# Performance work log

Hardware: AMD Instinct MI355X
Metric: run time of the kernel (lower is better)

Reference implementation:

```python
import jax, jax.numpy as jnp
import numpy as np

# hyperparameters (match init_kwargs / AF3 atom transformer)
B, N, C, CP = 1, 2048, 128, 16      # batch, n_atom, c_atom, c_atom_pair
H, D = 4, 32                        # heads, head dim
HD = H * D                          # 128
NB = 3                              # no_blocks
TC = 2 * C                          # n_transition * c_atom
NQ, NK = 32, 128                    # n_query, n_key
INF = 1.0e9


def _ln(x, g=None, b=None):
    m = jnp.mean(x, axis=-1, keepdims=True)
    v = jnp.mean((x - m) ** 2, axis=-1, keepdims=True)
    y = (x - m) * jax.lax.rsqrt(v + 1e-5)
    if g is not None:
        y = y * g
    if b is not None:
        y = y + b
    return y


def _adaln(a, s, gamma, wsig, bsig, wskip):
    # AF3 Algorithm 26: AdaLN(a, s)
    an = _ln(a)                     # no affine
    sn = _ln(s, gamma)              # scale only
    return jax.nn.sigmoid(sn @ wsig + bsig) * an + sn @ wskip


def _neighborhood_beta():
    # compute_neighborhood_mask with create_sparsity_mask=False
    n_center = N // NQ + 1
    centers = (NQ / 2 - 0.5) + jnp.arange(n_center, dtype=jnp.float32) * NQ
    l = jnp.arange(N, dtype=jnp.float32)
    row = (jnp.abs(l[:, None] - centers[None, :]) < NQ / 2).astype(jnp.float32)
    col = (jnp.abs(l[:, None] - centers[None, :]) < NK / 2).astype(jnp.float32)
    beta = row @ col.T              # [N, N], in {0,1} since query windows are disjoint
    return (beta - 1.0) * INF       # 0 where attended, -inf elsewhere


def setup_inputs() -> dict:
    key = jax.random.key(0)
    it = iter(jax.random.split(key, 64))
    def rn(shape, s=0.02):
        return jax.random.normal(next(it), shape, jnp.float32) * s
    inp = dict(
        ql=rn((B, N, C), 1.0),
        cl=rn((B, N, C), 1.0),
        plm=rn((B, N, N, CP), 1.0),
        atom_mask=jnp.ones((B, N), jnp.float32),
        # per-block stacked params, leading dim NB
        attn_gamma=1.0 + rn((NB, C)), attn_wsig=rn((NB, C, C)),
        attn_bsig=rn((NB, C)), attn_wskip=rn((NB, C, C)),
        wq=rn((NB, C, HD)), bq=rn((NB, HD)), wk=rn((NB, C, HD)), wv=rn((NB, C, HD)),
        lnz_g=1.0 + rn((NB, CP)), lnz_b=rn((NB, CP)), w_pair=rn((NB, CP, H)),
        w_gate=rn((NB, C, HD)), w_out=rn((NB, HD, C)),
        w_ao=rn((NB, C, C)), b_ao=rn((NB, C)) - 2.0,
        tr_gamma=1.0 + rn((NB, C)), tr_wsig=rn((NB, C, C)),
        tr_bsig=rn((NB, C)), tr_wskip=rn((NB, C, C)),
        w_t1=rn((NB, C, TC)), w_t2=rn((NB, C, TC)), w_t3=rn((NB, TC, C)),
        w_to=rn((NB, C, C)), b_to=rn((NB, C)) - 2.0,
    )
    return inp


def reference(ql, cl, plm, atom_mask,
              attn_gamma, attn_wsig, attn_bsig, attn_wskip,
              wq, bq, wk, wv, lnz_g, lnz_b, w_pair,
              w_gate, w_out, w_ao, b_ao,
              tr_gamma, tr_wsig, tr_bsig, tr_wskip,
              w_t1, w_t2, w_t3, w_to, b_to):
    beta = _neighborhood_beta()                       # [N, N]
    mask_bias = (atom_mask - 1.0) * INF               # [B, N]
    scale = 1.0 / np.sqrt(D)
    a, s = ql, cl
    for i in range(NB):
        # --- AttentionPairBias with AdaLN (AF3 Alg. 24) ---
        an = _adaln(a, s, attn_gamma[i], attn_wsig[i], attn_bsig[i], attn_wskip[i])
        q = (an @ wq[i] + bq[i]).reshape(B, N, H, D)
        k = (an @ wk[i]).reshape(B, N, H, D)
        v = (an @ wv[i]).reshape(B, N, H, D)
        pb = _ln(plm, lnz_g[i], lnz_b[i]) @ w_pair[i]  # [B, N, N, H]
        logits = (jnp.einsum('bqhd,bkhd->bhqk', q, k) * scale
                  + pb.transpose(0, 3, 1, 2)
                  + beta[None, None]
                  + mask_bias[:, None, None, :])
        attn = jax.nn.softmax(logits, axis=-1)
        o = jnp.einsum('bhqk,bkhd->bqhd', attn, v)
        g = jax.nn.sigmoid(an @ w_gate[i]).reshape(B, N, H, D)
        o = (g * o).reshape(B, N, HD) @ w_out[i]
        b_attn = jax.nn.sigmoid(s @ w_ao[i] + b_ao[i]) * o   # adaLN-zero output gate
        # --- ConditionedTransitionBlock (AF3 Alg. 25) on old a ---
        tn = _adaln(a, s, tr_gamma[i], tr_wsig[i], tr_bsig[i], tr_wskip[i])
        t = jax.nn.silu(tn @ w_t1[i]) * (tn @ w_t2[i])       # SwiGLU
        t = jax.nn.sigmoid(s @ w_to[i] + b_to[i]) * (t @ w_t3[i])
        a = b_attn + t                                       # AF3 Alg. 23
    return a
```

## Files before the change

kernel.cpp:

```cpp
#include <hip/hip_runtime.h>
#include <math.h>

#define NA 2048
#define CD 128
#define NC ((size_t)262144)

typedef unsigned short u16;
typedef short s8v __attribute__((ext_vector_type(8)));
typedef float f4v __attribute__((ext_vector_type(4)));

__device__ __forceinline__ float sigm(float x) { return 1.f / (1.f + __expf(-x)); }

__device__ __forceinline__ u16 f2bf(float x) {
    unsigned u = __float_as_uint(x);
    u += 0x7fffu + ((u >> 16) & 1u);
    return (u16)(u >> 16);
}
__device__ __forceinline__ float bf2f(u16 h) { return __uint_as_float((unsigned)h << 16); }

__global__ __launch_bounds__(256)
void prep_w(const float* __restrict__ attn_gamma, const float* __restrict__ attn_wsig,
            const float* __restrict__ attn_bsig, const float* __restrict__ attn_wskip,
            const float* __restrict__ wq, const float* __restrict__ wk,
            const float* __restrict__ wv, const float* __restrict__ w_gate,
            const float* __restrict__ w_out, const float* __restrict__ w_ao,
            const float* __restrict__ b_ao,
            const float* __restrict__ tr_gamma, const float* __restrict__ tr_wsig,
            const float* __restrict__ tr_bsig, const float* __restrict__ tr_wskip,
            const float* __restrict__ w_t1, const float* __restrict__ w_t2,
            const float* __restrict__ w_t3, const float* __restrict__ w_to,
            const float* __restrict__ b_to,
            u16* __restrict__ BP1h, u16* __restrict__ BP1l,
            u16* __restrict__ BG1h, u16* __restrict__ BG1l,
            u16* __restrict__ BG2h, u16* __restrict__ BG2l,
            float* __restrict__ Pbias) {
    int e = blockIdx.x * 256 + threadIdx.x;
    if (e >= 835584) {
        int t = e - 835584;
        if (t < 2304) {
            int z = t / 768, rem = t % 768, j = rem >> 7, c = rem & 127;
            float v = 0.f;
            if (j == 0) v = attn_bsig[z * 128 + c];
            else if (j == 2) v = tr_bsig[z * 128 + c];
            else if (j == 4) v = b_ao[z * 128 + c];
            else if (j == 5) v = b_to[z * 128 + c];
            Pbias[t] = v;
        }
        return;
    }
    int z = e / 278528, r = e % 278528;
    float val;
    u16 *dh, *dl;
    size_t dofs;
    if (r < 98304) {
        int c = r >> 7, k = r & 127, seg = c >> 7, cc = c & 127;
        const float* w;
        const float* g = nullptr;
        switch (seg) {
            case 0: w = attn_wsig; g = attn_gamma; break;
            case 1: w = attn_wskip; g = attn_gamma; break;
            case 2: w = tr_wsig; g = tr_gamma; break;
            case 3: w = tr_wskip; g = tr_gamma; break;
            case 4: w = w_ao; break;
            default: w = w_to; break;
        }
        val = w[((size_t)z * 128 + k) * 128 + cc];
        if (g) val *= g[z * 128 + k];
        dh = BP1h; dl = BP1l; dofs = (size_t)z * 98304 + r;
    } else if (r < 229376) {
        int t = r - 98304, c = t >> 7, k = t & 127;
        if (c < 512) {
            int seg = c >> 7, cc = c & 127;
            const float* w = (seg == 0) ? wq : (seg == 1) ? wk : (seg == 2) ? wv : w_gate;
            val = w[((size_t)z * 128 + k) * 128 + cc];
        } else {
            int tt = c - 512;
            const float* w = (tt < 256) ? w_t1 : w_t2;
            val = w[(size_t)z * 32768 + (size_t)k * 256 + (tt & 255)];
        }
        dh = BG1h; dl = BG1l; dofs = (size_t)z * 131072 + t;
    } else {
        int t = r - 229376, c = t / 384, k = t % 384;
        val = (k < 128) ? w_out[((size_t)z * 128 + k) * 128 + c]
                        : w_t3[(size_t)z * 32768 + (size_t)(k - 128) * 128 + c];
        dh = BG2h; dl = BG2l; dofs = (size_t)z * 49152 + t;
    }
    u16 h = f2bf(val);
    dh[dofs] = h;
    dl[dofs] = f2bf(val - bf2f(h));
}

__global__ __launch_bounds__(256)
void ln_split(const float* __restrict__ cl, u16* __restrict__ lnsh, u16* __restrict__ lnsl,
              u16* __restrict__ clh, u16* __restrict__ cll) {
    int row = blockIdx.x * 4 + (threadIdx.x >> 6);
    int lane = threadIdx.x & 63;
    size_t idx = (size_t)row * CD + lane * 2;
    float2 v = *(const float2*)(cl + idx);
    float s = v.x + v.y, sq = v.x * v.x + v.y * v.y;
#pragma unroll
    for (int m = 1; m < 64; m <<= 1) { s += __shfl_xor(s, m); sq += __shfl_xor(sq, m); }
    float mean = s * (1.f / 128.f);
    float var = sq * (1.f / 128.f) - mean * mean;
    float r = 1.f / sqrtf(var + 1e-5f);
    float lx = (v.x - mean) * r, ly = (v.y - mean) * r;
    ushort2 h, l;
    h.x = f2bf(lx); h.y = f2bf(ly);
    l.x = f2bf(lx - bf2f(h.x)); l.y = f2bf(ly - bf2f(h.y));
    *(ushort2*)(lnsh + idx) = h; *(ushort2*)(lnsl + idx) = l;
    h.x = f2bf(v.x); h.y = f2bf(v.y);
    l.x = f2bf(v.x - bf2f(h.x)); l.y = f2bf(v.y - bf2f(h.y));
    *(ushort2*)(clh + idx) = h; *(ushort2*)(cll + idx) = l;
}

__global__ __launch_bounds__(256)
void an_tn(const float* __restrict__ a, const float* __restrict__ sg,
           u16* __restrict__ anh, u16* __restrict__ anl,
           u16* __restrict__ tnh, u16* __restrict__ tnl) {
    int row = blockIdx.x * 4 + (threadIdx.x >> 6);
    int lane = threadIdx.x & 63;
    size_t idx = (size_t)row * CD + lane * 2;
    float2 v = *(const float2*)(a + idx);
    float s = v.x + v.y, sq = v.x * v.x + v.y * v.y;
#pragma unroll
    for (int m = 1; m < 64; m <<= 1) { s += __shfl_xor(s, m); sq += __shfl_xor(sq, m); }
    float mean = s * (1.f / 128.f);
    float var = sq * (1.f / 128.f) - mean * mean;
    float r = 1.f / sqrtf(var + 1e-5f);
    float lx = (v.x - mean) * r, ly = (v.y - mean) * r;
    float2 s0 = *(const float2*)(sg + idx);
    float2 s1 = *(const float2*)(sg + NC + idx);
    float2 s2 = *(const float2*)(sg + 2 * NC + idx);
    float2 s3 = *(const float2*)(sg + 3 * NC + idx);
    float ax = fmaf(s0.x, lx, s1.x), ay = fmaf(s0.y, ly, s1.y);
    float tx = fmaf(s2.x, lx, s3.x), ty = fmaf(s2.y, ly, s3.y);
    ushort2 h, l;
    h.x = f2bf(ax); h.y = f2bf(ay);
    l.x = f2bf(ax - bf2f(h.x)); l.y = f2bf(ay - bf2f(h.y));
    *(ushort2*)(anh + idx) = h; *(ushort2*)(anl + idx) = l;
    h.x = f2bf(tx); h.y = f2bf(ty);
    l.x = f2bf(tx - bf2f(h.x)); l.y = f2bf(ty - bf2f(h.y));
    *(ushort2*)(tnh + idx) = h; *(ushort2*)(tnl + idx) = l;
}

__device__ __forceinline__ void mf_core(const u16* __restrict__ Ah, const u16* __restrict__ Al,
                                        int AK, int kA,
                                        const u16* __restrict__ Bh, const u16* __restrict__ Bl,
                                        int BK, int kB,
                                        int r0, int c0, int nks, f4v (&acc)[2][2]) {
    const int lane = threadIdx.x & 63;
    const int lr = lane & 15;
    const int kg = (lane >> 4) << 3;
    const u16* pa = Ah + (size_t)(r0 + lr) * AK + kA + kg;
    const u16* pal = Al + (size_t)(r0 + lr) * AK + kA + kg;
    const u16* pb = Bh + (size_t)(c0 + lr) * BK + kB + kg;
    const u16* pbl = Bl + (size_t)(c0 + lr) * BK + kB + kg;
    const size_t aS = (size_t)16 * AK, bS = (size_t)16 * BK;
#pragma unroll
    for (int ks = 0; ks < nks; ++ks) {
        const int ko = ks * 32;
        s8v a0h = *(const s8v*)(pa + ko);
        s8v a1h = *(const s8v*)(pa + aS + ko);
        s8v a0l = *(const s8v*)(pal + ko);
        s8v a1l = *(const s8v*)(pal + aS + ko);
        s8v b0h = *(const s8v*)(pb + ko);
        s8v b1h = *(const s8v*)(pb + bS + ko);
        s8v b0l = *(const s8v*)(pbl + ko);
        s8v b1l = *(const s8v*)(pbl + bS + ko);
        acc[0][0] = __builtin_amdgcn_mfma_f32_16x16x32_bf16(a0h, b0h, acc[0][0], 0, 0, 0);
        acc[0][1] = __builtin_amdgcn_mfma_f32_16x16x32_bf16(a0h, b1h, acc[0][1], 0, 0, 0);
        acc[1][0] = __builtin_amdgcn_mfma_f32_16x16x32_bf16(a1h, b0h, acc[1][0], 0, 0, 0);
        acc[1][1] = __builtin_amdgcn_mfma_f32_16x16x32_bf16(a1h, b1h, acc[1][1], 0, 0, 0);
        acc[0][0] = __builtin_amdgcn_mfma_f32_16x16x32_bf16(a0h, b0l, acc[0][0], 0, 0, 0);
        acc[0][1] = __builtin_amdgcn_mfma_f32_16x16x32_bf16(a0h, b1l, acc[0][1], 0, 0, 0);
        acc[1][0] = __builtin_amdgcn_mfma_f32_16x16x32_bf16(a1h, b0l, acc[1][0], 0, 0, 0);
        acc[1][1] = __builtin_amdgcn_mfma_f32_16x16x32_bf16(a1h, b1l, acc[1][1], 0, 0, 0);
        acc[0][0] = __builtin_amdgcn_mfma_f32_16x16x32_bf16(a0l, b0h, acc[0][0], 0, 0, 0);
        acc[0][1] = __builtin_amdgcn_mfma_f32_16x16x32_bf16(a0l, b1h, acc[0][1], 0, 0, 0);
        acc[1][0] = __builtin_amdgcn_mfma_f32_16x16x32_bf16(a1l, b0h, acc[1][0], 0, 0, 0);
        acc[1][1] = __builtin_amdgcn_mfma_f32_16x16x32_bf16(a1l, b1h, acc[1][1], 0, 0, 0);
    }
}

__global__ __launch_bounds__(256)
void mf_p1(const u16* __restrict__ lnsh, const u16* __restrict__ lnsl,
           const u16* __restrict__ clh, const u16* __restrict__ cll,
           const u16* __restrict__ BP1h, const u16* __restrict__ BP1l,
           const float* __restrict__ Pbias, float* __restrict__ sg) {
    const int z = blockIdx.z, chunk = blockIdx.y;
    const int r0 = blockIdx.x * 32;
    const int c0 = (threadIdx.x >> 6) * 32;
    const u16* Ah = (chunk < 4) ? lnsh : clh;
    const u16* Al = (chunk < 4) ? lnsl : cll;
    const size_t bo = (size_t)z * 98304 + (size_t)chunk * 16384;
    f4v acc[2][2] = {};
    mf_core(Ah, Al, 128, 0, BP1h + bo, BP1l + bo, 128, 0, r0, c0, 4, acc);
    const bool dosig = (chunk != 1) && (chunk != 3);
    const float* bp = Pbias + (z * 6 + chunk) * 128;
    float* dst = sg + ((size_t)z * 6 + chunk) * NC;
    const int lane = threadIdx.x & 63;
    const int lr = lane & 15, rb = (lane >> 4) * 4;
#pragma unroll
    for (int mi = 0; mi < 2; ++mi)
#pragma unroll
        for (int i = 0; i < 4; ++i) {
            int row = r0 + mi * 16 + rb + i;
#pragma unroll
            for (int ni = 0; ni < 2; ++ni) {
                int col = c0 + ni * 16 + lr;
                float x = acc[mi][ni][i];
                if (dosig) x = sigm(x + bp[col]);
                dst[(size_t)row * CD + col] = x;
            }
        }
}

__global__ __launch_bounds__(256)
void mf_g1(const u16* __restrict__ anh, const u16* __restrict__ anl,
           const u16* __restrict__ tnh, const u16* __restrict__ tnl,
           const u16* __restrict__ Bh, const u16* __restrict__ Bl,
           const float* __restrict__ bq, float* __restrict__ qkvg, float* __restrict__ tbuf) {
    const int chunk = blockIdx.y;
    const int r0 = blockIdx.x * 32;
    const int c0 = (threadIdx.x >> 6) * 32;
    const u16* Ah = (chunk < 4) ? anh : tnh;
    const u16* Al = (chunk < 4) ? anl : tnl;
    const size_t bo = (size_t)chunk * 16384;
    f4v acc[2][2] = {};
    mf_core(Ah, Al, 128, 0, Bh + bo, Bl + bo, 128, 0, r0, c0, 4, acc);
    float* dst;
    int cb;
    if (chunk < 4) { dst = qkvg; cb = chunk * 128; } else { dst = tbuf; cb = (chunk - 4) * 128; }
    const int lane = threadIdx.x & 63;
    const int lr = lane & 15, rb = (lane >> 4) * 4;
#pragma unroll
    for (int mi = 0; mi < 2; ++mi)
#pragma unroll
        for (int i = 0; i < 4; ++i) {
            int row = r0 + mi * 16 + rb + i;
#pragma unroll
            for (int ni = 0; ni < 2; ++ni) {
                int col = c0 + ni * 16 + lr;
                float x = acc[mi][ni][i];
                if (chunk == 0) x += bq[col];
                dst[(size_t)row * 512 + cb + col] = x;
            }
        }
}

__global__ __launch_bounds__(256)
void mf_g2(const u16* __restrict__ ogh, const u16* __restrict__ ogl,
           const u16* __restrict__ swh, const u16* __restrict__ swl,
           const u16* __restrict__ Bh, const u16* __restrict__ Bl,
           const float* __restrict__ sg4, const float* __restrict__ sg5,
           float* __restrict__ dst) {
    const int r0 = blockIdx.x * 32;
    const int c0 = (threadIdx.x >> 6) * 32;
    f4v acc1[2][2] = {}, acc2[2][2] = {};
    mf_core(ogh, ogl, 128, 0, Bh, Bl, 384, 0, r0, c0, 4, acc1);
    mf_core(swh, swl, 256, 0, Bh, Bl, 384, 128, r0, c0, 8, acc2);
    const int lane = threadIdx.x & 63;
    const int lr = lane & 15, rb = (lane >> 4) * 4;
#pragma unroll
    for (int mi = 0; mi < 2; ++mi)
#pragma unroll
        for (int i = 0; i < 4; ++i) {
            int row = r0 + mi * 16 + rb + i;
#pragma unroll
            for (int ni = 0; ni < 2; ++ni) {
                int col = c0 + ni * 16 + lr;
                size_t idx = (size_t)row * CD + col;
                dst[idx] = sg4[idx] * acc1[mi][ni][i] + sg5[idx] * acc2[mi][ni][i];
            }
        }
}

__global__ __launch_bounds__(256)
void pb_kernel(const float* __restrict__ plm, const float* __restrict__ lnz_g,
               const float* __restrict__ lnz_b, const float* __restrict__ w_pair,
               float* __restrict__ pb) {
    __shared__ float gw[3][4][16];
    __shared__ float c0[3][4];
    int t = threadIdx.x;
    if (t < 12) {
        int i = t >> 2, h = t & 3;
        float c = 0.f;
        for (int cp = 0; cp < 16; ++cp) {
            float wp = w_pair[(i * 16 + cp) * 4 + h];
            gw[i][h][cp] = lnz_g[i * 16 + cp] * wp;
            c += lnz_b[i * 16 + cp] * wp;
        }
        c0[i][h] = c;
    }
    __syncthreads();
    int c = blockIdx.x;
    int p = blockIdx.y * 256 + t;
    int ql = p >> 7, kl = p & 127;
    int kstart = max(0, c * 32 - 48), kend = min(2048, c * 32 + 80);
    int k = kstart + kl;
    if (k >= kend) return;
    int q = c * 32 + ql;
    const float* row = plm + ((size_t)q * 2048 + (size_t)k) * 16;
    float x[16];
#pragma unroll
    for (int j = 0; j < 4; ++j) {
        float4 v = *(const float4*)(row + j * 4);
        x[j * 4 + 0] = v.x; x[j * 4 + 1] = v.y; x[j * 4 + 2] = v.z; x[j * 4 + 3] = v.w;
    }
    float s = 0.f, sq = 0.f;
#pragma unroll
    for (int cp = 0; cp < 16; ++cp) { s += x[cp]; sq += x[cp] * x[cp]; }
    float mean = s * (1.f / 16.f);
    float var = sq * (1.f / 16.f) - mean * mean;
    float r = 1.f / sqrtf(var + 1e-5f);
    float xn[16];
#pragma unroll
    for (int cp = 0; cp < 16; ++cp) xn[cp] = (x[cp] - mean) * r;
#pragma unroll
    for (int i = 0; i < 3; ++i)
#pragma unroll
        for (int h = 0; h < 4; ++h) {
            float d = c0[i][h];
#pragma unroll
            for (int cp = 0; cp < 16; ++cp) d = fmaf(xn[cp], gw[i][h][cp], d);
            pb[((((size_t)i * 64 + c) * 4 + h) * 32 + ql) * 128 + kl] = d;
        }
}

__global__ __launch_bounds__(256)
void attn_sw(const float* __restrict__ qkvg, const float* __restrict__ pb,
             const float* __restrict__ atom_mask, const float* __restrict__ tbuf,
             u16* __restrict__ ogh, u16* __restrict__ ogl,
             u16* __restrict__ swh, u16* __restrict__ swl) {
    const int c = blockIdx.x;
    const int tid = threadIdx.x;
    if (blockIdx.y >= 4) {
        const int r0 = c * 32;
        const int cb = (blockIdx.y - 4) * 128 + (tid & 31) * 4;
#pragma unroll
        for (int p = 0; p < 4; ++p) {
            int r = r0 + p * 8 + (tid >> 5);
            float4 x1 = *(const float4*)(tbuf + (size_t)r * 512 + cb);
            float4 x2 = *(const float4*)(tbuf + (size_t)r * 512 + 256 + cb);
            float4 s;
            s.x = x1.x * sigm(x1.x) * x2.x;
            s.y = x1.y * sigm(x1.y) * x2.y;
            s.z = x1.z * sigm(x1.z) * x2.z;
            s.w = x1.w * sigm(x1.w) * x2.w;
            size_t o = (size_t)r * 256 + cb;
            ushort4 h, l;
            h.x = f2bf(s.x); l.x = f2bf(s.x - bf2f(h.x));
            h.y = f2bf(s.y); l.y = f2bf(s.y - bf2f(h.y));
            h.z = f2bf(s.z); l.z = f2bf(s.z - bf2f(h.z));
            h.w = f2bf(s.w); l.w = f2bf(s.w - bf2f(h.w));
            *(ushort4*)(swh + o) = h;
            *(ushort4*)(swl + o) = l;
        }
        return;
    }
    const int h = blockIdx.y;
    const int kstart = max(0, c * 32 - 48);
    const int kend = min(2048, c * 32 + 80);
    const int nk = kend - kstart;

    __shared__ float Kt[128 * 36];
    __shared__ float Vt[128 * 36];
    __shared__ float Qs[32 * 36];
    __shared__ float Ps[32 * 132];

    {
        int q = tid >> 3, dq = tid & 7;
        float4 v = *(const float4*)(qkvg + (size_t)(c * 32 + q) * 512 + h * 32 + dq * 4);
        *(float4*)(Qs + q * 36 + dq * 4) = v;
    }
#pragma unroll
    for (int it = 0; it < 4; ++it) {
        int idx = it * 256 + tid;
        int kl = idx >> 3, dq = idx & 7;
        float4 kv = make_float4(0.f, 0.f, 0.f, 0.f);
        float4 vv = make_float4(0.f, 0.f, 0.f, 0.f);
        if (kl < nk) {
            size_t base = (size_t)(kstart + kl) * 512 + h * 32 + dq * 4;
            kv = *(const float4*)(qkvg + base + 128);
            vv = *(const float4*)(qkvg + base + 256);
        }
        int sw = (kl >> 4) & 7;
        *(float4*)(Kt + kl * 36 + ((dq ^ sw) << 2)) = kv;
        *(float4*)(Vt + kl * 36 + (dq << 2)) = vv;
    }
    __syncthreads();

    {
        const int qp = tid >> 4;
        const int ks = tid & 15;
        const int q0r = qp * 2, q1r = qp * 2 + 1;
        float4 qa[8], qb[8];
#pragma unroll
        for (int dq = 0; dq < 8; ++dq) {
            qa[dq] = *(const float4*)(Qs + q0r * 36 + dq * 4);
            qb[dq] = *(const float4*)(Qs + q1r * 36 + dq * 4);
        }
        const float* pbp = pb + ((size_t)(c * 4 + h) * 32) * 128;
        float lg0[8], lg1[8];
#pragma unroll
        for (int ki = 0; ki < 8; ++ki) {
            int kl = ks * 8 + ki;
            int sw = (kl >> 4) & 7;
            float d0 = 0.f, d1 = 0.f;
#pragma unroll
            for (int dq = 0; dq < 8; ++dq) {
                float4 kv = *(const float4*)(Kt + kl * 36 + ((dq ^ sw) << 2));
                d0 += qa[dq].x * kv.x + qa[dq].y * kv.y + qa[dq].z * kv.z + qa[dq].w * kv.w;
                d1 += qb[dq].x * kv.x + qb[dq].y * kv.y + qb[dq].z * kv.z + qb[dq].w * kv.w;
            }
            if (kl < nk) {
                int k = kstart + kl;
                float mb = (atom_mask[k] - 1.f) * 1.0e9f;
                lg0[ki] = fmaf(d0, 0.17677669529663687f, pbp[(size_t)q0r * 128 + kl] + mb);
                lg1[ki] = fmaf(d1, 0.17677669529663687f, pbp[(size_t)q1r * 128 + kl] + mb);
            } else {
                lg0[ki] = -1e30f;
                lg1[ki] = -1e30f;
            }
        }
        float m0 = lg0[0], m1 = lg1[0];
#pragma unroll
        for (int ki = 1; ki < 8; ++ki) { m0 = fmaxf(m0, lg0[ki]); m1 = fmaxf(m1, lg1[ki]); }
#pragma unroll
        for (int msk = 1; msk < 16; msk <<= 1) {
            m0 = fmaxf(m0, __shfl_xor(m0, msk));
            m1 = fmaxf(m1, __shfl_xor(m1, msk));
        }
        float s0 = 0.f, s1 = 0.f;
#pragma unroll
        for (int ki = 0; ki < 8; ++ki) {
            lg0[ki] = __expf(lg0[ki] - m0); s0 += lg0[ki];
            lg1[ki] = __expf(lg1[ki] - m1); s1 += lg1[ki];
        }
#pragma unroll
        for (int msk = 1; msk < 16; msk <<= 1) {
            s0 += __shfl_xor(s0, msk);
            s1 += __shfl_xor(s1, msk);
        }
        float i0 = 1.f / s0, i1 = 1.f / s1;
        float4 w;
        w.x = lg0[0] * i0; w.y = lg0[1] * i0; w.z = lg0[2] * i0; w.w = lg0[3] * i0;
        *(float4*)(Ps + q0r * 132 + ks * 8) = w;
        w.x = lg0[4] * i0; w.y = lg0[5] * i0; w.z = lg0[6] * i0; w.w = lg0[7] * i0;
        *(float4*)(Ps + q0r * 132 + ks * 8 + 4) = w;
        w.x = lg1[0] * i1; w.y = lg1[1] * i1; w.z = lg1[2] * i1; w.w = lg1[3] * i1;
        *(float4*)(Ps + q1r * 132 + ks * 8) = w;
        w.x = lg1[4] * i1; w.y = lg1[5] * i1; w.z = lg1[6] * i1; w.w = lg1[7] * i1;
        *(float4*)(Ps + q1r * 132 + ks * 8 + 4) = w;
    }
    __syncthreads();
    {
        const int q = tid >> 3;
        const int ds = tid & 7;
        float o0 = 0.f, o1 = 0.f, o2 = 0.f, o3 = 0.f;
#pragma unroll 4
        for (int kl = 0; kl < nk; ++kl) {
            float p = Ps[q * 132 + kl];
            float4 vv = *(const float4*)(Vt + kl * 36 + ds * 4);
            o0 = fmaf(p, vv.x, o0); o1 = fmaf(p, vv.y, o1);
            o2 = fmaf(p, vv.z, o2); o3 = fmaf(p, vv.w, o3);
        }
        size_t gl = (size_t)(c * 32 + q) * 512 + 384 + h * 32 + ds * 4;
        float4 g = *(const float4*)(qkvg + gl);
        float4 ov;
        ov.x = o0 * sigm(g.x); ov.y = o1 * sigm(g.y);
        ov.z = o2 * sigm(g.z); ov.w = o3 * sigm(g.w);
        size_t oidx = (size_t)(c * 32 + q) * 128 + h * 32 + ds * 4;
        ushort4 hh, ll;
        hh.x = f2bf(ov.x); ll.x = f2bf(ov.x - bf2f(hh.x));
        hh.y = f2bf(ov.y); ll.y = f2bf(ov.y - bf2f(hh.y));
        hh.z = f2bf(ov.z); ll.z = f2bf(ov.z - bf2f(hh.z));
        hh.w = f2bf(ov.w); ll.w = f2bf(ov.w - bf2f(hh.w));
        *(ushort4*)(ogh + oidx) = hh;
        *(ushort4*)(ogl + oidx) = ll;
    }
}

extern "C" void kernel_launch(void* const* d_in, const int* in_sizes, int n_in,
                              void* d_out, int out_size, void* d_ws, size_t ws_size,
                              hipStream_t stream) {
    const float* ql = (const float*)d_in[0];
    const float* cl = (const float*)d_in[1];
    const float* plm = (const float*)d_in[2];
    const float* atom_mask = (const float*)d_in[3];
    const float* attn_gamma = (const float*)d_in[4];
    const float* attn_wsig = (const float*)d_in[5];
    const float* attn_bsig = (const float*)d_in[6];
    const float* attn_wskip = (const float*)d_in[7];
    const float* wq = (const float*)d_in[8];
    const float* bq = (const float*)d_in[9];
    const float* wk = (const float*)d_in[10];
    const float* wv = (const float*)d_in[11];
    const float* lnz_g = (const float*)d_in[12];
    const float* lnz_b = (const float*)d_in[13];
    const float* w_pair = (const float*)d_in[14];
    const float* w_gate = (const float*)d_in[15];
    const float* w_out = (const float*)d_in[16];
    const float* w_ao = (const float*)d_in[17];
    const float* b_ao = (const float*)d_in[18];
    const float* tr_gamma = (const float*)d_in[19];
    const float* tr_wsig = (const float*)d_in[20];
    const float* tr_bsig = (const float*)d_in[21];
    const float* tr_wskip = (const float*)d_in[22];
    const float* w_t1 = (const float*)d_in[23];
    const float* w_t2 = (const float*)d_in[24];
    const float* w_t3 = (const float*)d_in[25];
    const float* w_to = (const float*)d_in[26];
    const float* b_to = (const float*)d_in[27];
    float* out = (float*)d_out;
    float* ws = (float*)d_ws;

    float* sg = ws;
    float* qkvg = ws + 18 * NC;
    float* tbuf = ws + 22 * NC;
    float* pb = ws + 26 * NC;
    float* a_buf = ws + 38 * NC;
    float* Pbias = ws + 39 * NC;
    u16* us = (u16*)(ws + 40 * NC);
    u16* lnsh = us;             u16* lnsl = us + NC;
    u16* clh = us + 2 * NC;     u16* cll = us + 3 * NC;
    u16* anh = us + 4 * NC;     u16* anl = us + 5 * NC;
    u16* tnh = us + 6 * NC;     u16* tnl = us + 7 * NC;
    u16* ogh = us + 8 * NC;     u16* ogl = us + 9 * NC;
    u16* swh = us + 10 * NC;    u16* swl = us + 12 * NC;
    u16* BP1h = us + 14 * NC;
    u16* BP1l = BP1h + 294912;
    u16* BG1h = BP1l + 294912;
    u16* BG1l = BG1h + 393216;
    u16* BG2h = BG1l + 393216;
    u16* BG2l = BG2h + 147456;

    prep_w<<<3273, 256, 0, stream>>>(attn_gamma, attn_wsig, attn_bsig, attn_wskip,
        wq, wk, wv, w_gate, w_out, w_ao, b_ao,
        tr_gamma, tr_wsig, tr_bsig, tr_wskip,
        w_t1, w_t2, w_t3, w_to, b_to,
        BP1h, BP1l, BG1h, BG1l, BG2h, BG2l, Pbias);
    ln_split<<<NA / 4, 256, 0, stream>>>(cl, lnsh, lnsl, clh, cll);
    mf_p1<<<dim3(64, 6, 3), 256, 0, stream>>>(lnsh, lnsl, clh, cll, BP1h, BP1l, Pbias, sg);
    pb_kernel<<<dim3(64, 16), 256, 0, stream>>>(plm, lnz_g, lnz_b, w_pair, pb);

    for (int i = 0; i < 3; ++i) {
        const float* a_cur = (i == 0) ? ql : a_buf;
        float* sgi = sg + (size_t)i * 6 * NC;
        an_tn<<<NA / 4, 256, 0, stream>>>(a_cur, sgi, anh, anl, tnh, tnl);
        mf_g1<<<dim3(64, 8), 256, 0, stream>>>(anh, anl, tnh, tnl,
            BG1h + (size_t)i * 131072, BG1l + (size_t)i * 131072,
            bq + (size_t)i * 128, qkvg, tbuf);
        attn_sw<<<dim3(64, 6), 256, 0, stream>>>(qkvg,
            pb + (size_t)i * 64 * 4 * 32 * 128, atom_mask, tbuf, ogh, ogl, swh, swl);
        float* dst = (i == 2) ? out : a_buf;
        mf_g2<<<64, 256, 0, stream>>>(ogh, ogl, swh, swl,
            BG2h + (size_t)i * 49152, BG2l + (size_t)i * 49152,
            sgi + 4 * NC, sgi + 5 * NC, dst);
    }
}
```

Before: 163.4 us.

## Fuse LayerNorm into GEMMs, move attention to MFMA, fuse SwiGLU into output GEMM

Folds the LayerNorm/AdaLN and bf16 hi/lo split into the GEMM kernels through swizzled LDS staging, removing the separate ln_split and an_tn passes. Attention is rewritten to use MFMA on bf16-split Q and transposed V, and the SwiGLU product is computed inside the output GEMM. pb_kernel now writes zeros for out-of-range keys. A hipMemsetAsync of the whole workspace is added each call, which brings extra memory traffic.

```diff
diff --git a/kernel.cpp b/kernel.cpp
--- a/kernel.cpp
+++ b/kernel.cpp
@@ -8,9 +8,9 @@
 typedef unsigned short u16;
 typedef short s8v __attribute__((ext_vector_type(8)));
 typedef float f4v __attribute__((ext_vector_type(4)));
+#define MFMA __builtin_amdgcn_mfma_f32_16x16x32_bf16
 
 __device__ __forceinline__ float sigm(float x) { return 1.f / (1.f + __expf(-x)); }
-
 __device__ __forceinline__ u16 f2bf(float x) {
     unsigned u = __float_as_uint(x);
     u += 0x7fffu + ((u >> 16) & 1u);
@@ -91,196 +91,11 @@
 }
 
 __global__ __launch_bounds__(256)
-void ln_split(const float* __restrict__ cl, u16* __restrict__ lnsh, u16* __restrict__ lnsl,
-              u16* __restrict__ clh, u16* __restrict__ cll) {
-    int row = blockIdx.x * 4 + (threadIdx.x >> 6);
-    int lane = threadIdx.x & 63;
-    size_t idx = (size_t)row * CD + lane * 2;
-    float2 v = *(const float2*)(cl + idx);
-    float s = v.x + v.y, sq = v.x * v.x + v.y * v.y;
-#pragma unroll
-    for (int m = 1; m < 64; m <<= 1) { s += __shfl_xor(s, m); sq += __shfl_xor(sq, m); }
-    float mean = s * (1.f / 128.f);
-    float var = sq * (1.f / 128.f) - mean * mean;
-    float r = 1.f / sqrtf(var + 1e-5f);
-    float lx = (v.x - mean) * r, ly = (v.y - mean) * r;
-    ushort2 h, l;
-    h.x = f2bf(lx); h.y = f2bf(ly);
-    l.x = f2bf(lx - bf2f(h.x)); l.y = f2bf(ly - bf2f(h.y));
-    *(ushort2*)(lnsh + idx) = h; *(ushort2*)(lnsl + idx) = l;
-    h.x = f2bf(v.x); h.y = f2bf(v.y);
-    l.x = f2bf(v.x - bf2f(h.x)); l.y = f2bf(v.y - bf2f(h.y));
-    *(ushort2*)(clh + idx) = h; *(ushort2*)(cll + idx) = l;
-}
-
-__global__ __launch_bounds__(256)
-void an_tn(const float* __restrict__ a, const float* __restrict__ sg,
-           u16* __restrict__ anh, u16* __restrict__ anl,
-           u16* __restrict__ tnh, u16* __restrict__ tnl) {
-    int row = blockIdx.x * 4 + (threadIdx.x >> 6);
-    int lane = threadIdx.x & 63;
-    size_t idx = (size_t)row * CD + lane * 2;
-    float2 v = *(const float2*)(a + idx);
-    float s = v.x + v.y, sq = v.x * v.x + v.y * v.y;
-#pragma unroll
-    for (int m = 1; m < 64; m <<= 1) { s += __shfl_xor(s, m); sq += __shfl_xor(sq, m); }
-    float mean = s * (1.f / 128.f);
-    float var = sq * (1.f / 128.f) - mean * mean;
-    float r = 1.f / sqrtf(var + 1e-5f);
-    float lx = (v.x - mean) * r, ly = (v.y - mean) * r;
-    float2 s0 = *(const float2*)(sg + idx);
-    float2 s1 = *(const float2*)(sg + NC + idx);
-    float2 s2 = *(const float2*)(sg + 2 * NC + idx);
-    float2 s3 = *(const float2*)(sg + 3 * NC + idx);
-    float ax = fmaf(s0.x, lx, s1.x), ay = fmaf(s0.y, ly, s1.y);
-    float tx = fmaf(s2.x, lx, s3.x), ty = fmaf(s2.y, ly, s3.y);
-    ushort2 h, l;
-    h.x = f2bf(ax); h.y = f2bf(ay);
-    l.x = f2bf(ax - bf2f(h.x)); l.y = f2bf(ay - bf2f(h.y));
-    *(ushort2*)(anh + idx) = h; *(ushort2*)(anl + idx) = l;
-    h.x = f2bf(tx); h.y = f2bf(ty);
-    l.x = f2bf(tx - bf2f(h.x)); l.y = f2bf(ty - bf2f(h.y));
-    *(ushort2*)(tnh + idx) = h; *(ushort2*)(tnl + idx) = l;
-}
-
-__device__ __forceinline__ void mf_core(const u16* __restrict__ Ah, const u16* __restrict__ Al,
-                                        int AK, int kA,
-                                        const u16* __restrict__ Bh, const u16* __restrict__ Bl,
-                                        int BK, int kB,
-                                        int r0, int c0, int nks, f4v (&acc)[2][2]) {
-    const int lane = threadIdx.x & 63;
-    const int lr = lane & 15;
-    const int kg = (lane >> 4) << 3;
-    const u16* pa = Ah + (size_t)(r0 + lr) * AK + kA + kg;
-    const u16* pal = Al + (size_t)(r0 + lr) * AK + kA + kg;
-    const u16* pb = Bh + (size_t)(c0 + lr) * BK + kB + kg;
-    const u16* pbl = Bl + (size_t)(c0 + lr) * BK + kB + kg;
-    const size_t aS = (size_t)16 * AK, bS = (size_t)16 * BK;
-#pragma unroll
-    for (int ks = 0; ks < nks; ++ks) {
-        const int ko = ks * 32;
-        s8v a0h = *(const s8v*)(pa + ko);
-        s8v a1h = *(const s8v*)(pa + aS + ko);
-        s8v a0l = *(const s8v*)(pal + ko);
-        s8v a1l = *(const s8v*)(pal + aS + ko);
-        s8v b0h = *(const s8v*)(pb + ko);
-        s8v b1h = *(const s8v*)(pb + bS + ko);
-        s8v b0l = *(const s8v*)(pbl + ko);
-        s8v b1l = *(const s8v*)(pbl + bS + ko);
-        acc[0][0] = __builtin_amdgcn_mfma_f32_16x16x32_bf16(a0h, b0h, acc[0][0], 0, 0, 0);
-        acc[0][1] = __builtin_amdgcn_mfma_f32_16x16x32_bf16(a0h, b1h, acc[0][1], 0, 0, 0);
-        acc[1][0] = __builtin_amdgcn_mfma_f32_16x16x32_bf16(a1h, b0h, acc[1][0], 0, 0, 0);
-        acc[1][1] = __builtin_amdgcn_mfma_f32_16x16x32_bf16(a1h, b1h, acc[1][1], 0, 0, 0);
-        acc[0][0] = __builtin_amdgcn_mfma_f32_16x16x32_bf16(a0h, b0l, acc[0][0], 0, 0, 0);
-        acc[0][1] = __builtin_amdgcn_mfma_f32_16x16x32_bf16(a0h, b1l, acc[0][1], 0, 0, 0);
-        acc[1][0] = __builtin_amdgcn_mfma_f32_16x16x32_bf16(a1h, b0l, acc[1][0], 0, 0, 0);
-        acc[1][1] = __builtin_amdgcn_mfma_f32_16x16x32_bf16(a1h, b1l, acc[1][1], 0, 0, 0);
-        acc[0][0] = __builtin_amdgcn_mfma_f32_16x16x32_bf16(a0l, b0h, acc[0][0], 0, 0, 0);
-        acc[0][1] = __builtin_amdgcn_mfma_f32_16x16x32_bf16(a0l, b1h, acc[0][1], 0, 0, 0);
-        acc[1][0] = __builtin_amdgcn_mfma_f32_16x16x32_bf16(a1l, b0h, acc[1][0], 0, 0, 0);
-        acc[1][1] = __builtin_amdgcn_mfma_f32_16x16x32_bf16(a1l, b1h, acc[1][1], 0, 0, 0);
-    }
-}
-
-__global__ __launch_bounds__(256)
-void mf_p1(const u16* __restrict__ lnsh, const u16* __restrict__ lnsl,
-           const u16* __restrict__ clh, const u16* __restrict__ cll,
-           const u16* __restrict__ BP1h, const u16* __restrict__ BP1l,
-           const float* __restrict__ Pbias, float* __restrict__ sg) {
-    const int z = blockIdx.z, chunk = blockIdx.y;
-    const int r0 = blockIdx.x * 32;
-    const int c0 = (threadIdx.x >> 6) * 32;
-    const u16* Ah = (chunk < 4) ? lnsh : clh;
-    const u16* Al = (chunk < 4) ? lnsl : cll;
-    const size_t bo = (size_t)z * 98304 + (size_t)chunk * 16384;
-    f4v acc[2][2] = {};
-    mf_core(Ah, Al, 128, 0, BP1h + bo, BP1l + bo, 128, 0, r0, c0, 4, acc);
-    const bool dosig = (chunk != 1) && (chunk != 3);
-    const float* bp = Pbias + (z * 6 + chunk) * 128;
-    float* dst = sg + ((size_t)z * 6 + chunk) * NC;
-    const int lane = threadIdx.x & 63;
-    const int lr = lane & 15, rb = (lane >> 4) * 4;
-#pragma unroll
-    for (int mi = 0; mi < 2; ++mi)
-#pragma unroll
-        for (int i = 0; i < 4; ++i) {
-            int row = r0 + mi * 16 + rb + i;
-#pragma unroll
-            for (int ni = 0; ni < 2; ++ni) {
-                int col = c0 + ni * 16 + lr;
-                float x = acc[mi][ni][i];
-                if (dosig) x = sigm(x + bp[col]);
-                dst[(size_t)row * CD + col] = x;
-            }
-        }
-}
-
-__global__ __launch_bounds__(256)
-void mf_g1(const u16* __restrict__ anh, const u16* __restrict__ anl,
-           const u16* __restrict__ tnh, const u16* __restrict__ tnl,
-           const u16* __restrict__ Bh, const u16* __restrict__ Bl,
-           const float* __restrict__ bq, float* __restrict__ qkvg, float* __restrict__ tbuf) {
-    const int chunk = blockIdx.y;
-    const int r0 = blockIdx.x * 32;
-    const int c0 = (threadIdx.x >> 6) * 32;
-    const u16* Ah = (chunk < 4) ? anh : tnh;
-    const u16* Al = (chunk < 4) ? anl : tnl;
-    const size_t bo = (size_t)chunk * 16384;
-    f4v acc[2][2] = {};
-    mf_core(Ah, Al, 128, 0, Bh + bo, Bl + bo, 128, 0, r0, c0, 4, acc);
-    float* dst;
-    int cb;
-    if (chunk < 4) { dst = qkvg; cb = chunk * 128; } else { dst = tbuf; cb = (chunk - 4) * 128; }
-    const int lane = threadIdx.x & 63;
-    const int lr = lane & 15, rb = (lane >> 4) * 4;
-#pragma unroll
-    for (int mi = 0; mi < 2; ++mi)
-#pragma unroll
-        for (int i = 0; i < 4; ++i) {
-            int row = r0 + mi * 16 + rb + i;
-#pragma unroll
-            for (int ni = 0; ni < 2; ++ni) {
-                int col = c0 + ni * 16 + lr;
-                float x = acc[mi][ni][i];
-                if (chunk == 0) x += bq[col];
-                dst[(size_t)row * 512 + cb + col] = x;
-            }
-        }
-}
-
-__global__ __launch_bounds__(256)
-void mf_g2(const u16* __restrict__ ogh, const u16* __restrict__ ogl,
-           const u16* __restrict__ swh, const u16* __restrict__ swl,
-           const u16* __restrict__ Bh, const u16* __restrict__ Bl,
-           const float* __restrict__ sg4, const float* __restrict__ sg5,
-           float* __restrict__ dst) {
-    const int r0 = blockIdx.x * 32;
-    const int c0 = (threadIdx.x >> 6) * 32;
-    f4v acc1[2][2] = {}, acc2[2][2] = {};
-    mf_core(ogh, ogl, 128, 0, Bh, Bl, 384, 0, r0, c0, 4, acc1);
-    mf_core(swh, swl, 256, 0, Bh, Bl, 384, 128, r0, c0, 8, acc2);
-    const int lane = threadIdx.x & 63;
-    const int lr = lane & 15, rb = (lane >> 4) * 4;
-#pragma unroll
-    for (int mi = 0; mi < 2; ++mi)
-#pragma unroll
-        for (int i = 0; i < 4; ++i) {
-            int row = r0 + mi * 16 + rb + i;
-#pragma unroll
-            for (int ni = 0; ni < 2; ++ni) {
-                int col = c0 + ni * 16 + lr;
-                size_t idx = (size_t)row * CD + col;
-                dst[idx] = sg4[idx] * acc1[mi][ni][i] + sg5[idx] * acc2[mi][ni][i];
-            }
-        }
-}
-
-__global__ __launch_bounds__(256)
 void pb_kernel(const float* __restrict__ plm, const float* __restrict__ lnz_g,
                const float* __restrict__ lnz_b, const float* __restrict__ w_pair,
                float* __restrict__ pb) {
     __shared__ float gw[3][4][16];
-    __shared__ float c0[3][4];
+    __shared__ float c0s[3][4];
     int t = threadIdx.x;
     if (t < 12) {
         int i = t >> 2, h = t & 3;
@@ -290,7 +105,7 @@
             gw[i][h][cp] = lnz_g[i * 16 + cp] * wp;
             c += lnz_b[i * 16 + cp] * wp;
         }
-        c0[i][h] = c;
+        c0s[i][h] = c;
     }
     __syncthreads();
     int c = blockIdx.x;
@@ -298,7 +113,14 @@
     int ql = p >> 7, kl = p & 127;
     int kstart = max(0, c * 32 - 48), kend = min(2048, c * 32 + 80);
     int k = kstart + kl;
-    if (k >= kend) return;
+    if (k >= kend) {
+#pragma unroll
+        for (int i = 0; i < 3; ++i)
+#pragma unroll
+            for (int h = 0; h < 4; ++h)
+                pb[((((size_t)i * 64 + c) * 4 + h) * 32 + ql) * 128 + kl] = 0.f;
+        return;
+    }
     int q = c * 32 + ql;
     const float* row = plm + ((size_t)q * 2048 + (size_t)k) * 16;
     float x[16];
@@ -320,7 +142,7 @@
     for (int i = 0; i < 3; ++i)
 #pragma unroll
         for (int h = 0; h < 4; ++h) {
-            float d = c0[i][h];
+            float d = c0s[i][h];
 #pragma unroll
             for (int cp = 0; cp < 16; ++cp) d = fmaf(xn[cp], gw[i][h][cp], d);
             pb[((((size_t)i * 64 + c) * 4 + h) * 32 + ql) * 128 + kl] = d;
@@ -328,157 +150,400 @@
 }
 
 __global__ __launch_bounds__(256)
-void attn_sw(const float* __restrict__ qkvg, const float* __restrict__ pb,
-             const float* __restrict__ atom_mask, const float* __restrict__ tbuf,
-             u16* __restrict__ ogh, u16* __restrict__ ogl,
-             u16* __restrict__ swh, u16* __restrict__ swl) {
-    const int c = blockIdx.x;
-    const int tid = threadIdx.x;
-    if (blockIdx.y >= 4) {
-        const int r0 = c * 32;
-        const int cb = (blockIdx.y - 4) * 128 + (tid & 31) * 4;
-#pragma unroll
-        for (int p = 0; p < 4; ++p) {
-            int r = r0 + p * 8 + (tid >> 5);
-            float4 x1 = *(const float4*)(tbuf + (size_t)r * 512 + cb);
-            float4 x2 = *(const float4*)(tbuf + (size_t)r * 512 + 256 + cb);
-            float4 s;
-            s.x = x1.x * sigm(x1.x) * x2.x;
-            s.y = x1.y * sigm(x1.y) * x2.y;
-            s.z = x1.z * sigm(x1.z) * x2.z;
-            s.w = x1.w * sigm(x1.w) * x2.w;
-            size_t o = (size_t)r * 256 + cb;
-            ushort4 h, l;
-            h.x = f2bf(s.x); l.x = f2bf(s.x - bf2f(h.x));
-            h.y = f2bf(s.y); l.y = f2bf(s.y - bf2f(h.y));
-            h.z = f2bf(s.z); l.z = f2bf(s.z - bf2f(h.z));
-            h.w = f2bf(s.w); l.w = f2bf(s.w - bf2f(h.w));
-            *(ushort4*)(swh + o) = h;
-            *(ushort4*)(swl + o) = l;
-        }
-        return;
-    }
-    const int h = blockIdx.y;
+void mf_p1f(const float* __restrict__ cl, const u16* __restrict__ B1h, const u16* __restrict__ B1l,
+            const float* __restrict__ Pbias, float* __restrict__ sg) {
+    const int r0 = blockIdx.x * 32, chunk = blockIdx.y, z = blockIdx.z;
+    __shared__ u16 Ah[32 * 128], Al[32 * 128];
+    {
+        const int tid = threadIdx.x;
+        const int row = tid >> 3, cb = (tid & 7) * 16;
+        const float* ar = cl + (size_t)(r0 + row) * CD + cb;
+        float x[16];
+#pragma unroll
+        for (int j = 0; j < 4; ++j) {
+            float4 v = *(const float4*)(ar + j * 4);
+            x[4 * j] = v.x; x[4 * j + 1] = v.y; x[4 * j + 2] = v.z; x[4 * j + 3] = v.w;
+        }
+        float s = 0.f, sq = 0.f;
+#pragma unroll
+        for (int j = 0; j < 16; ++j) { s += x[j]; sq += x[j] * x[j]; }
+#pragma unroll
+        for (int m = 1; m < 8; m <<= 1) { s += __shfl_xor(s, m); sq += __shfl_xor(sq, m); }
+        float mean = s * (1.f / 128.f), var = sq * (1.f / 128.f) - mean * mean;
+        float rr = 1.f / sqrtf(var + 1e-5f);
+#pragma unroll
+        for (int gp = 0; gp < 2; ++gp) {
+            u16 hv8[8], lv8[8];
+#pragma unroll
+            for (int j = 0; j < 8; ++j) {
+                float xv = x[gp * 8 + j];
+                float val = (chunk < 4) ? (xv - mean) * rr : xv;
+                u16 hh = f2bf(val);
+                hv8[j] = hh; lv8[j] = f2bf(val - bf2f(hh));
+            }
+            int g = ((cb >> 3) + gp) ^ (row & 7);
+            *(s8v*)(Ah + row * 128 + g * 8) = *(s8v*)hv8;
+            *(s8v*)(Al + row * 128 + g * 8) = *(s8v*)lv8;
+        }
+    }
+    __syncthreads();
+    const int l = threadIdx.x & 63, w = threadIdx.x >> 6;
+    const int lr = l & 15, lq = l >> 4, kg = lq * 8;
+    const int c0 = w * 32;
+    const u16* Bh = B1h + (size_t)z * 98304 + (size_t)chunk * 16384;
+    const u16* Bl = B1l + (size_t)z * 98304 + (size_t)chunk * 16384;
+    f4v acc[2][2] = {};
+#pragma unroll
+    for (int ks = 0; ks < 4; ++ks) {
+        int g = (4 * ks + lq) ^ (lr & 7);
+        s8v a0h = *(const s8v*)(Ah + lr * 128 + g * 8);
+        s8v a1h = *(const s8v*)(Ah + (16 + lr) * 128 + g * 8);
+        s8v a0l = *(const s8v*)(Al + lr * 128 + g * 8);
+        s8v a1l = *(const s8v*)(Al + (16 + lr) * 128 + g * 8);
+        s8v b0h = *(const s8v*)(Bh + (size_t)(c0 + lr) * 128 + ks * 32 + kg);
+        s8v b1h = *(const s8v*)(Bh + (size_t)(c0 + 16 + lr) * 128 + ks * 32 + kg);
+        s8v b0l = *(const s8v*)(Bl + (size_t)(c0 + lr) * 128 + ks * 32 + kg);
+        s8v b1l = *(const s8v*)(Bl + (size_t)(c0 + 16 + lr) * 128 + ks * 32 + kg);
+        acc[0][0] = MFMA(a0h, b0h, acc[0][0], 0, 0, 0); acc[0][1] = MFMA(a0h, b1h, acc[0][1], 0, 0, 0);
+        acc[1][0] = MFMA(a1h, b0h, acc[1][0], 0, 0, 0); acc[1][1] = MFMA(a1h, b1h, acc[1][1], 0, 0, 0);
+        acc[0][0] = MFMA(a0h, b0l, acc[0][0], 0, 0, 0); acc[0][1] = MFMA(a0h, b1l, acc[0][1], 0, 0, 0);
+        acc[1][0] = MFMA(a1h, b0l, acc[1][0], 0, 0, 0); acc[1][1] = MFMA(a1h, b1l, acc[1][1], 0, 0, 0);
+        acc[0][0] = MFMA(a0l, b0h, acc[0][0], 0, 0, 0); acc[0][1] = MFMA(a0l, b1h, acc[0][1], 0, 0, 0);
+        acc[1][0] = MFMA(a1l, b0h, acc[1][0], 0, 0, 0); acc[1][1] = MFMA(a1l, b1h, acc[1][1], 0, 0, 0);
+    }
+    const bool dosig = (chunk != 1) && (chunk != 3);
+    const float* bp = Pbias + (z * 6 + chunk) * 128;
+    float* dst = sg + ((size_t)z * 6 + chunk) * NC;
+#pragma unroll
+    for (int mi = 0; mi < 2; ++mi)
+#pragma unroll
+        for (int i = 0; i < 4; ++i) {
+            int row = r0 + mi * 16 + lq * 4 + i;
+#pragma unroll
+            for (int ni = 0; ni < 2; ++ni) {
+                int col = c0 + ni * 16 + lr;
+                float xx = acc[mi][ni][i];
+                if (dosig) xx = sigm(xx + bp[col]);
+                dst[(size_t)row * CD + col] = xx;
+            }
+        }
+}
+
+__global__ __launch_bounds__(256)
+void k1_fused(const float* __restrict__ a, const float* __restrict__ sgi,
+              const u16* __restrict__ B1h, const u16* __restrict__ B1l,
+              const float* __restrict__ bq,
+              u16* __restrict__ qgh, u16* __restrict__ qgl,
+              u16* __restrict__ vTh, u16* __restrict__ vTl,
+              float* __restrict__ tbuf) {
+    const int r0 = blockIdx.x * 32;
+    const int y = blockIdx.y;
+    __shared__ u16 Ah[32 * 128], Al[32 * 128];
+    {
+        const int tid = threadIdx.x;
+        const int row = tid >> 3, cb = (tid & 7) * 16;
+        const float* ar = a + (size_t)(r0 + row) * CD + cb;
+        float x[16];
+#pragma unroll
+        for (int j = 0; j < 4; ++j) {
+            float4 v = *(const float4*)(ar + j * 4);
+            x[4 * j] = v.x; x[4 * j + 1] = v.y; x[4 * j + 2] = v.z; x[4 * j + 3] = v.w;
+        }
+        float s = 0.f, sq = 0.f;
+#pragma unroll
+        for (int j = 0; j < 16; ++j) { s += x[j]; sq += x[j] * x[j]; }
+#pragma unroll
+        for (int m = 1; m < 8; m <<= 1) { s += __shfl_xor(s, m); sq += __shfl_xor(sq, m); }
+        float mean = s * (1.f / 128.f), var = sq * (1.f / 128.f) - mean * mean;
+        float rr = 1.f / sqrtf(var + 1e-5f);
+        const float* sig = sgi + ((y < 2) ? 0 : 2 * NC) + (size_t)(r0 + row) * CD + cb;
+        const float* skp = sgi + ((y < 2) ? NC : 3 * NC) + (size_t)(r0 + row) * CD + cb;
+#pragma unroll
+        for (int gp = 0; gp < 2; ++gp) {
+            u16 hv8[8], lv8[8];
+#pragma unroll
+            for (int j = 0; j < 8; ++j) {
+                int jj = gp * 8 + j;
+                float ln = (x[jj] - mean) * rr;
+                float val = fmaf(sig[jj], ln, skp[jj]);
+                u16 hh = f2bf(val);
+                hv8[j] = hh; lv8[j] = f2bf(val - bf2f(hh));
+            }
+            int g = ((cb >> 3) + gp) ^ (row & 7);
+            *(s8v*)(Ah + row * 128 + g * 8) = *(s8v*)hv8;
+            *(s8v*)(Al + row * 128 + g * 8) = *(s8v*)lv8;
+        }
+    }
+    __syncthreads();
+    const int l = threadIdx.x & 63, w = threadIdx.x >> 6;
+    const int lr = l & 15, lq = l >> 4, kg = lq * 8;
+    const int chunk = 2 * y + (w >> 1);
+    const int cbase = (w & 1) * 64;
+    f4v acc[2][2][2] = {};
+#pragma unroll
+    for (int ks = 0; ks < 4; ++ks) {
+        int g = (4 * ks + lq) ^ (lr & 7);
+        s8v a0h = *(const s8v*)(Ah + lr * 128 + g * 8);
+        s8v a1h = *(const s8v*)(Ah + (16 + lr) * 128 + g * 8);
+        s8v a0l = *(const s8v*)(Al + lr * 128 + g * 8);
+        s8v a1l = *(const s8v*)(Al + (16 + lr) * 128 + g * 8);
+#pragma unroll
+        for (int t2 = 0; t2 < 2; ++t2) {
+            int crow = chunk * 128 + cbase + t2 * 32;
+            s8v b0h = *(const s8v*)(B1h + (size_t)(crow + lr) * 128 + ks * 32 + kg);
+            s8v b1h = *(const s8v*)(B1h + (size_t)(crow + 16 + lr) * 128 + ks * 32 + kg);
+            s8v b0l = *(const s8v*)(B1l + (size_t)(crow + lr) * 128 + ks * 32 + kg);
+            s8v b1l = *(const s8v*)(B1l + (size_t)(crow + 16 + lr) * 128 + ks * 32 + kg);
+            acc[t2][0][0] = MFMA(a0h, b0h, acc[t2][0][0], 0, 0, 0);
+            acc[t2][0][1] = MFMA(a0h, b1h, acc[t2][0][1], 0, 0, 0);
+            acc[t2][1][0] = MFMA(a1h, b0h, acc[t2][1][0], 0, 0, 0);
+            acc[t2][1][1] = MFMA(a1h, b1h, acc[t2][1][1], 0, 0, 0);
+            acc[t2][0][0] = MFMA(a0h, b0l, acc[t2][0][0], 0, 0, 0);
+            acc[t2][0][1] = MFMA(a0h, b1l, acc[t2][0][1], 0, 0, 0);
+            acc[t2][1][0] = MFMA(a1h, b0l, acc[t2][1][0], 0, 0, 0);
+            acc[t2][1][1] = MFMA(a1h, b1l, acc[t2][1][1], 0, 0, 0);
+            acc[t2][0][0] = MFMA(a0l, b0h, acc[t2][0][0], 0, 0, 0);
+            acc[t2][0][1] = MFMA(a0l, b1h, acc[t2][0][1], 0, 0, 0);
+            acc[t2][1][0] = MFMA(a1l, b0h, acc[t2][1][0], 0, 0, 0);
+            acc[t2][1][1] = MFMA(a1l, b1h, acc[t2][1][1], 0, 0, 0);
+        }
+    }
+#pragma unroll
+    for (int t2 = 0; t2 < 2; ++t2)
+#pragma unroll
+        for (int mi = 0; mi < 2; ++mi)
+#pragma unroll
+            for (int i = 0; i < 4; ++i) {
+                int row = r0 + mi * 16 + lq * 4 + i;
+#pragma unroll
+                for (int ni = 0; ni < 2; ++ni) {
+                    int gcol = chunk * 128 + cbase + t2 * 32 + ni * 16 + lr;
+                    float x = acc[t2][mi][ni][i];
+                    if (chunk == 0) x += bq[gcol];
+                    if (gcol < 512) {
+                        u16 hh = f2bf(x), ll = f2bf(x - bf2f(hh));
+                        qgh[(size_t)row * 512 + gcol] = hh;
+                        qgl[(size_t)row * 512 + gcol] = ll;
+                        if (chunk == 2) {
+                            int cv = gcol - 256;
+                            vTh[(size_t)cv * 2048 + row] = hh;
+                            vTl[(size_t)cv * 2048 + row] = ll;
+                        }
+                    } else {
+                        tbuf[(size_t)row * 512 + (gcol - 512)] = x;
+                    }
+                }
+            }
+}
+
+__global__ __launch_bounds__(64)
+void attn_mfma(const u16* __restrict__ qgh, const u16* __restrict__ qgl,
+               const u16* __restrict__ vTh, const u16* __restrict__ vTl,
+               const float* __restrict__ pb, const float* __restrict__ atom_mask,
+               u16* __restrict__ ogh, u16* __restrict__ ogl) {
+    const int c = blockIdx.x, h = blockIdx.y;
+    const int l = threadIdx.x;
     const int kstart = max(0, c * 32 - 48);
     const int kend = min(2048, c * 32 + 80);
     const int nk = kend - kstart;
-
-    __shared__ float Kt[128 * 36];
-    __shared__ float Vt[128 * 36];
-    __shared__ float Qs[32 * 36];
-    __shared__ float Ps[32 * 132];
-
+    const int lr = l & 15, lq = l >> 4, kg = lq * 8;
+
+    __shared__ u16 Pls[32 * 128];
+
+    s8v qfh[2], qfl[2];
+#pragma unroll
+    for (int mi = 0; mi < 2; ++mi) {
+        size_t qb = (size_t)(c * 32 + mi * 16 + lr) * 512 + h * 32 + kg;
+        qfh[mi] = *(const s8v*)(qgh + qb);
+        qfl[mi] = *(const s8v*)(qgl + qb);
+    }
+    f4v lac[2][8] = {};
+#pragma unroll
+    for (int kt = 0; kt < 8; ++kt) {
+        int krow = min(kstart + kt * 16 + lr, 2047);
+        size_t kb = (size_t)krow * 512 + 128 + h * 32 + kg;
+        s8v bh = *(const s8v*)(qgh + kb);
+        s8v bl = *(const s8v*)(qgl + kb);
+        lac[0][kt] = MFMA(qfh[0], bh, lac[0][kt], 0, 0, 0);
+        lac[1][kt] = MFMA(qfh[1], bh, lac[1][kt], 0, 0, 0);
+        lac[0][kt] = MFMA(qfh[0], bl, lac[0][kt], 0, 0, 0);
+        lac[1][kt] = MFMA(qfh[1], bl, lac[1][kt], 0, 0, 0);
+        lac[0][kt] = MFMA(qfl[0], bh, lac[0][kt], 0, 0, 0);
+        lac[1][kt] = MFMA(qfl[1], bh, lac[1][kt], 0, 0, 0);
+    }
+    float mb8[8];
+#pragma unroll
+    for (int kt = 0; kt < 8; ++kt) {
+        int kl = kt * 16 + lr;
+        mb8[kt] = (kl < nk) ? (atom_mask[kstart + kl] - 1.f) * 1.0e9f : 0.f;
+    }
+    const float scale = 0.17677669529663687f;
+    const float* pbp = pb + (size_t)((c * 4 + h) * 32) * 128;
+    float inv_s[2][4];
+#pragma unroll
+    for (int mi = 0; mi < 2; ++mi)
+#pragma unroll
+        for (int i = 0; i < 4; ++i) {
+            const int rl = mi * 16 + lq * 4 + i;
+            float lg[8];
+#pragma unroll
+            for (int kt = 0; kt < 8; ++kt) {
+                int kl = kt * 16 + lr;
+                float v = -1e30f;
+                if (kl < nk) v = fmaf(lac[mi][kt][i], scale, pbp[(size_t)rl * 128 + kl] + mb8[kt]);
+                lg[kt] = v;
+            }
+            float m = lg[0];
+#pragma unroll
+            for (int kt = 1; kt < 8; ++kt) m = fmaxf(m, lg[kt]);
+#pragma unroll
+            for (int msk = 1; msk < 16; msk <<= 1) m = fmaxf(m, __shfl_xor(m, msk));
+            float ssum = 0.f;
+#pragma unroll
+            for (int kt = 0; kt < 8; ++kt) {
+                float p = __expf(lg[kt] - m);
+                u16 p16 = f2bf(p);
+                ssum += bf2f(p16);
+                int kl = kt * 16 + lr;
+                int g = (kl >> 3) ^ (rl & 7);
+                Pls[rl * 128 + g * 8 + (kl & 7)] = p16;
+            }
+#pragma unroll
+            for (int msk = 1; msk < 16; msk <<= 1) ssum += __shfl_xor(ssum, msk);
+            inv_s[mi][i] = 1.f / ssum;
+        }
+    __syncthreads();
+    f4v oac[2][2] = {};
+#pragma unroll
+    for (int ks = 0; ks < 4; ++ks) {
+        s8v pA[2];
+#pragma unroll
+        for (int mi = 0; mi < 2; ++mi) {
+            int row = mi * 16 + lr;
+            int g = (4 * ks + lq) ^ (row & 7);
+            pA[mi] = *(const s8v*)(Pls + row * 128 + g * 8);
+        }
+#pragma unroll
+        for (int ct = 0; ct < 2; ++ct) {
+            size_t vb = (size_t)(h * 32 + ct * 16 + lr) * 2048 + kstart + ks * 32 + kg;
+            s8v vh = *(const s8v*)(vTh + vb);
+            s8v vl = *(const s8v*)(vTl + vb);
+            oac[0][ct] = MFMA(pA[0], vh, oac[0][ct], 0, 0, 0);
+            oac[1][ct] = MFMA(pA[1], vh, oac[1][ct], 0, 0, 0);
+            oac[0][ct] = MFMA(pA[0], vl, oac[0][ct], 0, 0, 0);
+            oac[1][ct] = MFMA(pA[1], vl, oac[1][ct], 0, 0, 0);
+        }
+    }
+#pragma unroll
+    for (int mi = 0; mi < 2; ++mi)
+#pragma unroll
+        for (int ct = 0; ct < 2; ++ct)
+#pragma unroll
+            for (int i = 0; i < 4; ++i) {
+                int rl = mi * 16 + lq * 4 + i;
+                int row = c * 32 + rl;
+                int d = ct * 16 + lr;
+                float o = oac[mi][ct][i] * inv_s[mi][i];
+                size_t gidx = (size_t)row * 512 + 384 + h * 32 + d;
+                float g = bf2f(qgh[gidx]) + bf2f(qgl[gidx]);
+                float v = o * sigm(g);
+                u16 hh = f2bf(v);
+                size_t oi = (size_t)row * 128 + h * 32 + d;
+                ogh[oi] = hh;
+                ogl[oi] = f2bf(v - bf2f(hh));
+            }
+}
+
+__global__ __launch_bounds__(256)
+void k3_fused(const float* __restrict__ tbuf,
+              const u16* __restrict__ ogh, const u16* __restrict__ ogl,
+              const u16* __restrict__ B2h, const u16* __restrict__ B2l,
+              const float* __restrict__ sg4, const float* __restrict__ sg5,
+              float* __restrict__ dst) {
+    const int r0 = blockIdx.x * 32;
+    __shared__ u16 Sh[32 * 256], Sl[32 * 256];
     {
-        int q = tid >> 3, dq = tid & 7;
-        float4 v = *(const float4*)(qkvg + (size_t)(c * 32 + q) * 512 + h * 32 + dq * 4);
-        *(float4*)(Qs + q * 36 + dq * 4) = v;
-    }
-#pragma unroll
-    for (int it = 0; it < 4; ++it) {
-        int idx = it * 256 + tid;
-        int kl = idx >> 3, dq = idx & 7;
-        float4 kv = make_float4(0.f, 0.f, 0.f, 0.f);
-        float4 vv = make_float4(0.f, 0.f, 0.f, 0.f);
-        if (kl < nk) {
-            size_t base = (size_t)(kstart + kl) * 512 + h * 32 + dq * 4;
-            kv = *(const float4*)(qkvg + base + 128);
-            vv = *(const float4*)(qkvg + base + 256);
-        }
-        int sw = (kl >> 4) & 7;
-        *(float4*)(Kt + kl * 36 + ((dq ^ sw) << 2)) = kv;
-        *(float4*)(Vt + kl * 36 + (dq << 2)) = vv;
+        const int tid = threadIdx.x;
+        const int row = tid >> 3, cb = (tid & 7) * 32;
+#pragma unroll
+        for (int u = 0; u < 4; ++u) {
+            int colb = cb + u * 8;
+            const float* t1 = tbuf + (size_t)(r0 + row) * 512 + colb;
+            const float* t2 = t1 + 256;
+            u16 hv8[8], lv8[8];
+#pragma unroll
+            for (int j2 = 0; j2 < 2; ++j2) {
+                float4 x1 = *(const float4*)(t1 + j2 * 4);
+                float4 x2 = *(const float4*)(t2 + j2 * 4);
+                float sv[4];
+                sv[0] = x1.x * sigm(x1.x) * x2.x;
+                sv[1] = x1.y * sigm(x1.y) * x2.y;
+                sv[2] = x1.z * sigm(x1.z) * x2.z;
+                sv[3] = x1.w * sigm(x1.w) * x2.w;
+#pragma unroll
+                for (int j = 0; j < 4; ++j) {
+                    u16 hh = f2bf(sv[j]);
+                    hv8[j2 * 4 + j] = hh;
+                    lv8[j2 * 4 + j] = f2bf(sv[j] - bf2f(hh));
+                }
+            }
+            int g = (colb >> 3) ^ (row & 7);
+            *(s8v*)(Sh + row * 256 + g * 8) = *(s8v*)hv8;
+            *(s8v*)(Sl + row * 256 + g * 8) = *(s8v*)lv8;
+        }
     }
     __syncthreads();
-
-    {
-        const int qp = tid >> 4;
-        const int ks = tid & 15;
-        const int q0r = qp * 2, q1r = qp * 2 + 1;
-        float4 qa[8], qb[8];
-#pragma unroll
-        for (int dq = 0; dq < 8; ++dq) {
-            qa[dq] = *(const float4*)(Qs + q0r * 36 + dq * 4);
-            qb[dq] = *(const float4*)(Qs + q1r * 36 + dq * 4);
-        }
-        const float* pbp = pb + ((size_t)(c * 4 + h) * 32) * 128;
-        float lg0[8], lg1[8];
-#pragma unroll
-        for (int ki = 0; ki < 8; ++ki) {
-            int kl = ks * 8 + ki;
-            int sw = (kl >> 4) & 7;
-            float d0 = 0.f, d1 = 0.f;
-#pragma unroll
-            for (int dq = 0; dq < 8; ++dq) {
-                float4 kv = *(const float4*)(Kt + kl * 36 + ((dq ^ sw) << 2));
-                d0 += qa[dq].x * kv.x + qa[dq].y * kv.y + qa[dq].z * kv.z + qa[dq].w * kv.w;
-                d1 += qb[dq].x * kv.x + qb[dq].y * kv.y + qb[dq].z * kv.z + qb[dq].w * kv.w;
-            }
-            if (kl < nk) {
-                int k = kstart + kl;
-                float mb = (atom_mask[k] - 1.f) * 1.0e9f;
-                lg0[ki] = fmaf(d0, 0.17677669529663687f, pbp[(size_t)q0r * 128 + kl] + mb);
-                lg1[ki] = fmaf(d1, 0.17677669529663687f, pbp[(size_t)q1r * 128 + kl] + mb);
-            } else {
-                lg0[ki] = -1e30f;
-                lg1[ki] = -1e30f;
-            }
-        }
-        float m0 = lg0[0], m1 = lg1[0];
-#pragma unroll
-        for (int ki = 1; ki < 8; ++ki) { m0 = fmaxf(m0, lg0[ki]); m1 = fmaxf(m1, lg1[ki]); }
-#pragma unroll
-        for (int msk = 1; msk < 16; msk <<= 1) {
-            m0 = fmaxf(m0, __shfl_xor(m0, msk));
-            m1 = fmaxf(m1, __shfl_xor(m1, msk));
-        }
-        float s0 = 0.f, s1 = 0.f;
-#pragma unroll
-        for (int ki = 0; ki < 8; ++ki) {
-            lg0[ki] = __expf(lg0[ki] - m0); s0 += lg0[ki];
-            lg1[ki] = __expf(lg1[ki] - m1); s1 += lg1[ki];
-        }
-#pragma unroll
-        for (int msk = 1; msk < 16; msk <<= 1) {
-            s0 += __shfl_xor(s0, msk);
-            s1 += __shfl_xor(s1, msk);
-        }
-        float i0 = 1.f / s0, i1 = 1.f / s1;
-        float4 w;
-        w.x = lg0[0] * i0; w.y = lg0[1] * i0; w.z = lg0[2] * i0; w.w = lg0[3] * i0;
-        *(float4*)(Ps + q0r * 132 + ks * 8) = w;
-        w.x = lg0[4] * i0; w.y = lg0[5] * i0; w.z = lg0[6] * i0; w.w = lg0[7] * i0;
-        *(float4*)(Ps + q0r * 132 + ks * 8 + 4) = w;
-        w.x = lg1[0] * i1; w.y = lg1[1] * i1; w.z = lg1[2] * i1; w.w = lg1[3] * i1;
-        *(float4*)(Ps + q1r * 132 + ks * 8) = w;
-        w.x = lg1[4] * i1; w.y = lg1[5] * i1; w.z = lg1[6] * i1; w.w = lg1[7] * i1;
-        *(float4*)(Ps + q1r * 132 + ks * 8 + 4) = w;
-    }
-    __syncthreads();
-    {
-        const int q = tid >> 3;
-        const int ds = tid & 7;
-        float o0 = 0.f, o1 = 0.f, o2 = 0.f, o3 = 0.f;
-#pragma unroll 4
-        for (int kl = 0; kl < nk; ++kl) {
-            float p = Ps[q * 132 + kl];
-            float4 vv = *(const float4*)(Vt + kl * 36 + ds * 4);
-            o0 = fmaf(p, vv.x, o0); o1 = fmaf(p, vv.y, o1);
-            o2 = fmaf(p, vv.z, o2); o3 = fmaf(p, vv.w, o3);
-        }
-        size_t gl = (size_t)(c * 32 + q) * 512 + 384 + h * 32 + ds * 4;
-        float4 g = *(const float4*)(qkvg + gl);
-        float4 ov;
-        ov.x = o0 * sigm(g.x); ov.y = o1 * sigm(g.y);
-        ov.z = o2 * sigm(g.z); ov.w = o3 * sigm(g.w);
-        size_t oidx = (size_t)(c * 32 + q) * 128 + h * 32 + ds * 4;
-        ushort4 hh, ll;
-        hh.x = f2bf(ov.x); ll.x = f2bf(ov.x - bf2f(hh.x));
-        hh.y = f2bf(ov.y); ll.y = f2bf(ov.y - bf2f(hh.y));
-        hh.z = f2bf(ov.z); ll.z = f2bf(ov.z - bf2f(hh.z));
-        hh.w = f2bf(ov.w); ll.w = f2bf(ov.w - bf2f(hh.w));
-        *(ushort4*)(ogh + oidx) = hh;
-        *(ushort4*)(ogl + oidx) = ll;
-    }
+    const int l = threadIdx.x & 63, w = threadIdx.x >> 6;
+    const int lr = l & 15, lq = l >> 4, kg = lq * 8;
+    const int c0 = w * 32;
+    f4v ac1[2][2] = {}, ac2[2][2] = {};
+#pragma unroll
+    for (int ks = 0; ks < 4; ++ks) {
+        s8v a0h = *(const s8v*)(ogh + (size_t)(r0 + lr) * 128 + ks * 32 + kg);
+        s8v a1h = *(const s8v*)(ogh + (size_t)(r0 + 16 + lr) * 128 + ks * 32 + kg);
+        s8v a0l = *(const s8v*)(ogl + (size_t)(r0 + lr) * 128 + ks * 32 + kg);
+        s8v a1l = *(const s8v*)(ogl + (size_t)(r0 + 16 + lr) * 128 + ks * 32 + kg);
+        s8v b0h = *(const s8v*)(B2h + (size_t)(c0 + lr) * 384 + ks * 32 + kg);
+        s8v b1h = *(const s8v*)(B2h + (size_t)(c0 + 16 + lr) * 384 + ks * 32 + kg);
+        s8v b0l = *(const s8v*)(B2l + (size_t)(c0 + lr) * 384 + ks * 32 + kg);
+        s8v b1l = *(const s8v*)(B2l + (size_t)(c0 + 16 + lr) * 384 + ks * 32 + kg);
+        ac1[0][0] = MFMA(a0h, b0h, ac1[0][0], 0, 0, 0); ac1[0][1] = MFMA(a0h, b1h, ac1[0][1], 0, 0, 0);
+        ac1[1][0] = MFMA(a1h, b0h, ac1[1][0], 0, 0, 0); ac1[1][1] = MFMA(a1h, b1h, ac1[1][1], 0, 0, 0);
+        ac1[0][0] = MFMA(a0h, b0l, ac1[0][0], 0, 0, 0); ac1[0][1] = MFMA(a0h, b1l, ac1[0][1], 0, 0, 0);
+        ac1[1][0] = MFMA(a1h, b0l, ac1[1][0], 0, 0, 0); ac1[1][1] = MFMA(a1h, b1l, ac1[1][1], 0, 0, 0);
+        ac1[0][0] = MFMA(a0l, b0h, ac1[0][0], 0, 0, 0); ac1[0][1] = MFMA(a0l, b1h, ac1[0][1], 0, 0, 0);
+        ac1[1][0] = MFMA(a1l, b0h, ac1[1][0], 0, 0, 0); ac1[1][1] = MFMA(a1l, b1h, ac1[1][1], 0, 0, 0);
+    }
+#pragma unroll
+    for (int ks = 0; ks < 8; ++ks) {
+        int g = (4 * ks + lq) ^ (lr & 7);
+        s8v a0h = *(const s8v*)(Sh + lr * 256 + g * 8);
+        s8v a1h = *(const s8v*)(Sh + (16 + lr) * 256 + g * 8);
+        s8v a0l = *(const s8v*)(Sl + lr * 256 + g * 8);
+        s8v a1l = *(const s8v*)(Sl + (16 + lr) * 256 + g * 8);
+        s8v b0h = *(const s8v*)(B2h + (size_t)(c0 + lr) * 384 + 128 + ks * 32 + kg);
+        s8v b1h = *(const s8v*)(B2h + (size_t)(c0 + 16 + lr) * 384 + 128 + ks * 32 + kg);
+        s8v b0l = *(const s8v*)(B2l + (size_t)(c0 + lr) * 384 + 128 + ks * 32 + kg);
+        s8v b1l = *(const s8v*)(B2l + (size_t)(c0 + 16 + lr) * 384 + 128 + ks * 32 + kg);
+        ac2[0][0] = MFMA(a0h, b0h, ac2[0][0], 0, 0, 0); ac2[0][1] = MFMA(a0h, b1h, ac2[0][1], 0, 0, 0);
+        ac2[1][0] = MFMA(a1h, b0h, ac2[1][0], 0, 0, 0); ac2[1][1] = MFMA(a1h, b1h, ac2[1][1], 0, 0, 0);
+        ac2[0][0] = MFMA(a0h, b0l, ac2[0][0], 0, 0, 0); ac2[0][1] = MFMA(a0h, b1l, ac2[0][1], 0, 0, 0);
+        ac2[1][0] = MFMA(a1h, b0l, ac2[1][0], 0, 0, 0); ac2[1][1] = MFMA(a1h, b1l, ac2[1][1], 0, 0, 0);
+        ac2[0][0] = MFMA(a0l, b0h, ac2[0][0], 0, 0, 0); ac2[0][1] = MFMA(a0l, b1h, ac2[0][1], 0, 0, 0);
+        ac2[1][0] = MFMA(a1l, b0h, ac2[1][0], 0, 0, 0); ac2[1][1] = MFMA(a1l, b1h, ac2[1][1], 0, 0, 0);
+    }
+#pragma unroll
+    for (int mi = 0; mi < 2; ++mi)
+#pragma unroll
+        for (int i = 0; i < 4; ++i) {
+            int row = r0 + mi * 16 + lq * 4 + i;
+#pragma unroll
+            for (int ni = 0; ni < 2; ++ni) {
+                int col = c0 + ni * 16 + lr;
+                size_t idx = (size_t)row * CD + col;
+                dst[idx] = sg4[idx] * ac1[mi][ni][i] + sg5[idx] * ac2[mi][ni][i];
+            }
+        }
 }
 
 extern "C" void kernel_launch(void* const* d_in, const int* in_sizes, int n_in,
@@ -516,45 +581,46 @@
     float* ws = (float*)d_ws;
 
     float* sg = ws;
-    float* qkvg = ws + 18 * NC;
-    float* tbuf = ws + 22 * NC;
-    float* pb = ws + 26 * NC;
-    float* a_buf = ws + 38 * NC;
-    float* Pbias = ws + 39 * NC;
-    u16* us = (u16*)(ws + 40 * NC);
-    u16* lnsh = us;             u16* lnsl = us + NC;
-    u16* clh = us + 2 * NC;     u16* cll = us + 3 * NC;
-    u16* anh = us + 4 * NC;     u16* anl = us + 5 * NC;
-    u16* tnh = us + 6 * NC;     u16* tnl = us + 7 * NC;
-    u16* ogh = us + 8 * NC;     u16* ogl = us + 9 * NC;
-    u16* swh = us + 10 * NC;    u16* swl = us + 12 * NC;
-    u16* BP1h = us + 14 * NC;
+    float* tbuf = ws + 18 * NC;
+    float* pb = ws + 22 * NC;
+    float* a_buf = ws + 34 * NC;
+    float* Pbias = ws + 35 * NC;
+    u16* us = (u16*)(ws + 36 * NC);
+    u16* qgh = us;
+    u16* qgl = qgh + 4 * NC;
+    u16* ogh = qgl + 4 * NC;
+    u16* ogl = ogh + NC;
+    u16* vTh = ogl + NC;
+    u16* vTl = vTh + NC + 128;
+    u16* BP1h = vTl + NC + 128;
     u16* BP1l = BP1h + 294912;
     u16* BG1h = BP1l + 294912;
     u16* BG1l = BG1h + 393216;
     u16* BG2h = BG1l + 393216;
     u16* BG2l = BG2h + 147456;
 
+    size_t used_bytes = (size_t)36 * NC * 4 +
+                        ((size_t)12 * NC + 256 + 2 * 294912 + 2 * 393216 + 2 * 147456) * 2;
+    hipMemsetAsync(d_ws, 0, used_bytes, stream);
+
     prep_w<<<3273, 256, 0, stream>>>(attn_gamma, attn_wsig, attn_bsig, attn_wskip,
         wq, wk, wv, w_gate, w_out, w_ao, b_ao,
         tr_gamma, tr_wsig, tr_bsig, tr_wskip,
         w_t1, w_t2, w_t3, w_to, b_to,
         BP1h, BP1l, BG1h, BG1l, BG2h, BG2l, Pbias);
-    ln_split<<<NA / 4, 256, 0, stream>>>(cl, lnsh, lnsl, clh, cll);
-    mf_p1<<<dim3(64, 6, 3), 256, 0, stream>>>(lnsh, lnsl, clh, cll, BP1h, BP1l, Pbias, sg);
     pb_kernel<<<dim3(64, 16), 256, 0, stream>>>(plm, lnz_g, lnz_b, w_pair, pb);
+    mf_p1f<<<dim3(64, 6, 3), 256, 0, stream>>>(cl, BP1h, BP1l, Pbias, sg);
 
     for (int i = 0; i < 3; ++i) {
         const float* a_cur = (i == 0) ? ql : a_buf;
         float* sgi = sg + (size_t)i * 6 * NC;
-        an_tn<<<NA / 4, 256, 0, stream>>>(a_cur, sgi, anh, anl, tnh, tnl);
-        mf_g1<<<dim3(64, 8), 256, 0, stream>>>(anh, anl, tnh, tnl,
+        k1_fused<<<dim3(64, 4), 256, 0, stream>>>(a_cur, sgi,
             BG1h + (size_t)i * 131072, BG1l + (size_t)i * 131072,
-            bq + (size_t)i * 128, qkvg, tbuf);
-        attn_sw<<<dim3(64, 6), 256, 0, stream>>>(qkvg,
-            pb + (size_t)i * 64 * 4 * 32 * 128, atom_mask, tbuf, ogh, ogl, swh, swl);
+            bq + (size_t)i * 128, qgh, qgl, vTh, vTl, tbuf);
+        attn_mfma<<<dim3(64, 4), 64, 0, stream>>>(qgh, qgl, vTh, vTl,
+            pb + (size_t)i * 64 * 4 * 32 * 128, atom_mask, ogh, ogl);
         float* dst = (i == 2) ? out : a_buf;
-        mf_g2<<<64, 256, 0, stream>>>(ogh, ogl, swh, swl,
+        k3_fused<<<64, 256, 0, stream>>>(tbuf, ogh, ogl,
             BG2h + (size_t)i * 49152, BG2l + (size_t)i * 49152,
             sgi + 4 * NC, sgi + 5 * NC, dst);
     }
```

Measured after the change: 191.2 us. 1.17x slower.
